# Kernel optimization log

Measured on AMD Instinct MI355X. Metric: run time of the kernel, lower is better.

## Reference

```python
import jax, jax.numpy as jnp
import numpy as np

B, T, DIM, HEADS, DH = 4, 2048, 1024, 16, 64  # dh = dim // heads


def setup_inputs() -> dict:
    key = jax.random.key(0)
    k1, k2, k3 = jax.random.split(key, 3)
    x = jax.random.normal(k1, (B, T, DIM), dtype=jnp.float32)
    # nn.Linear weights, stored as [in, out] for x @ W convention
    W_qkv = jax.random.normal(k2, (DIM, 3 * HEADS * DH), dtype=jnp.float32) * (DIM ** -0.5)
    W_o = jax.random.normal(k3, (HEADS * DH, DIM), dtype=jnp.float32) * ((HEADS * DH) ** -0.5)
    return {"x": x, "W_qkv": W_qkv, "W_o": W_o}


def reference(x, W_qkv, W_o):
    b, t, _ = x.shape
    qkv = x @ W_qkv  # [b, t, 3*h*dh]
    # einops 'b t (d k h) -> k b h t d' with k=3, h=HEADS: fused axis splits as (dh, 3, h)
    qkv = qkv.reshape(b, t, DH, 3, HEADS)
    qkv = jnp.transpose(qkv, (3, 0, 4, 1, 2))  # [3, b, h, t, dh]
    q, k, v = qkv[0], qkv[1], qkv[2]
    scale = DH ** -0.5
    scores = jnp.einsum('bhid,bhjd->bhij', q, k) * scale  # [b, h, t, t]
    attn = jax.nn.softmax(scores, axis=-1)
    out = jnp.einsum('bhij,bhjd->bhid', attn, v)  # [b, h, t, dh]
    out = jnp.transpose(out, (0, 2, 1, 3)).reshape(b, t, HEADS * DH)  # 'b h t d -> b t (h d)'
    return out @ W_o
```

## Files before the change

kernel.cpp:

```cpp
#include <hip/hip_runtime.h>

typedef __bf16 bf16;
typedef __bf16 bf16x2 __attribute__((ext_vector_type(2)));
typedef __bf16 bf16x4 __attribute__((ext_vector_type(4)));
typedef __bf16 bf16x8 __attribute__((ext_vector_type(8)));
typedef float  f32x4  __attribute__((ext_vector_type(4)));
typedef unsigned int u32;
typedef unsigned int u32x2 __attribute__((ext_vector_type(2)));
typedef unsigned int u32x4 __attribute__((ext_vector_type(4)));

#define LOG2E 1.44269504088896340736f
#define EXP_SC (0.125f * LOG2E)

#if __has_builtin(__builtin_amdgcn_exp2f)
#define EXP2F(x) __builtin_amdgcn_exp2f(x)
#else
#define EXP2F(x) __builtin_exp2f(x)
#endif

__device__ __forceinline__ u32 pk_bf16(float lo, float hi) {
  u32 a = __float_as_uint(lo) + 0x8000u;
  u32 b = __float_as_uint(hi) + 0x8000u;
  return __builtin_amdgcn_perm(b, a, 0x07060302);
}
#if __has_builtin(__builtin_amdgcn_cvt_pk_bf16_f32)
__device__ __forceinline__ u32 cvtpk(float lo, float hi) {
  bf16x2 t = __builtin_amdgcn_cvt_pk_bf16_f32(lo, hi);
  return __builtin_bit_cast(u32, t);
}
#else
__device__ __forceinline__ u32 cvtpk(float lo, float hi) { return pk_bf16(lo, hi); }
#endif
__device__ __forceinline__ unsigned short bf16r(float x) {
  return (unsigned short)((__float_as_uint(x) + 0x8000u) >> 16);
}

__device__ __forceinline__ void async_ld16(void* lds, const void* g) {
  __builtin_amdgcn_global_load_lds(
      (const __attribute__((address_space(1))) void*)(g),
      (__attribute__((address_space(3))) void*)(lds),
      16, 0, 0);
}

__global__ void prep_all(const float* __restrict__ x,    bf16* __restrict__ xb,
                         const float* __restrict__ Wqkv, bf16* __restrict__ wqkvT,
                         const float* __restrict__ Wo,   bf16* __restrict__ woT) {
  __shared__ float s[12288];
  const int bid = blockIdx.x;
  const int tid = threadIdx.x;
  if (bid < 8192) {
    int i = bid * 256 + tid;
    float4 v = ((const float4*)x)[i];
    u32x2 o = { pk_bf16(v.x, v.y), pk_bf16(v.z, v.w) };
    *(u32x2*)(xb + (size_t)i * 4) = o;
  } else if (bid < 8448) {
    const int k0 = (bid - 8192) * 4;
    for (int i = tid; i < 3072; i += 256) {
      int r = i / 768, c = (i - r * 768) * 4;
      *(float4*)(s + r * 3072 + c) = *(const float4*)(Wqkv + (size_t)(k0 + r) * 3072 + c);
    }
    __syncthreads();
    for (int n = tid; n < 3072; n += 256) {
      int d = n & 63, h = (n >> 6) & 15, wch = n >> 10;
      int on = d * 48 + wch * 16 + h;
      u32x2 v = { pk_bf16(s[0 * 3072 + on], s[1 * 3072 + on]),
                  pk_bf16(s[2 * 3072 + on], s[3 * 3072 + on]) };
      *(u32x2*)(wqkvT + (size_t)n * 1024 + k0) = v;
    }
  } else {
    const int k0 = (bid - 8448) * 8;
    for (int i = tid; i < 2048; i += 256) {
      int r = i >> 8, c = (i & 255) * 4;
      *(float4*)(s + r * 1024 + c) = *(const float4*)(Wo + (size_t)(k0 + r) * 1024 + c);
    }
    __syncthreads();
    for (int n = tid; n < 1024; n += 256) {
      u32x4 v = { pk_bf16(s[0 * 1024 + n], s[1 * 1024 + n]),
                  pk_bf16(s[2 * 1024 + n], s[3 * 1024 + n]),
                  pk_bf16(s[4 * 1024 + n], s[5 * 1024 + n]),
                  pk_bf16(s[6 * 1024 + n], s[7 * 1024 + n]) };
      *(u32x4*)(woT + (size_t)n * 1024 + k0) = v;
    }
  }
}

template <int MODE>
__launch_bounds__(256, 2)
__global__ void gemm_bt(const bf16* __restrict__ A, const bf16* __restrict__ BT,
                        float* __restrict__ C, int N,
                        bf16* __restrict__ Qb, bf16* __restrict__ Kb, bf16* __restrict__ Vb) {
  constexpr int K = 1024;
  __shared__ bf16 sA[128 * 64];
  __shared__ bf16 sB[128 * 64];
  const int m0 = blockIdx.x * 128;
  const int n0 = blockIdx.y * 128;
  const int tid = threadIdx.x;
  const int lane = tid & 63;
  const int w = tid >> 6;
  const int wm = (w >> 1) * 64, wn = (w & 1) * 64;
  const int l15 = lane & 15, quad = lane >> 4;

  f32x4 acc[4][4];
  for (int i = 0; i < 4; i++)
    for (int j = 0; j < 4; j++) acc[i][j] = f32x4{0.f, 0.f, 0.f, 0.f};

  const int rT = tid >> 3;
  const int jT = (tid & 7) ^ (rT & 7);
  const bf16* gA = A  + (size_t)(m0 + rT) * K + jT * 8;
  const bf16* gB = BT + (size_t)(n0 + rT) * K + jT * 8;

  for (int k0 = 0; k0 < K; k0 += 64) {
    __syncthreads();
    for (int i = 0; i < 4; i++) {
      async_ld16((void*)(sA + (i * 256 + w * 64) * 8), gA + (size_t)i * 32 * K);
      async_ld16((void*)(sB + (i * 256 + w * 64) * 8), gB + (size_t)i * 32 * K);
    }
    gA += 64; gB += 64;
    __syncthreads();

    for (int kk = 0; kk < 2; kk++) {
      bf16x8 af[4], bfr[4];
      for (int ms = 0; ms < 4; ms++) {
        int r = wm + ms * 16 + l15;
        af[ms] = *(const bf16x8*)(sA + r * 64 + (((kk * 4 + quad) ^ (r & 7)) * 8));
      }
      for (int ns = 0; ns < 4; ns++) {
        int r = wn + ns * 16 + l15;
        bfr[ns] = *(const bf16x8*)(sB + r * 64 + (((kk * 4 + quad) ^ (r & 7)) * 8));
      }
      for (int ms = 0; ms < 4; ms++)
        for (int ns = 0; ns < 4; ns++)
          acc[ms][ns] = __builtin_amdgcn_mfma_f32_16x16x32_bf16(af[ms], bfr[ns], acc[ms][ns], 0, 0, 0);
    }
  }

  if (MODE == 0) {
    for (int ms = 0; ms < 4; ms++)
      for (int ns = 0; ns < 4; ns++)
        for (int r = 0; r < 4; r++) {
          int row = m0 + wm + ms * 16 + quad * 4 + r;
          int col = n0 + wn + ns * 16 + l15;
          C[(size_t)row * N + col] = acc[ms][ns][r];
        }
  } else {
    for (int ms = 0; ms < 4; ms++)
      for (int ns = 0; ns < 4; ns++)
        for (int r = 0; r < 4; r++) {
          int row = m0 + wm + ms * 16 + quad * 4 + r;
          int col = n0 + wn + ns * 16 + l15;
          int b = row >> 11, t = row & 2047;
          int d = col & 63, h = (col >> 6) & 15, wch = col >> 10;
          bf16* dst = (wch == 0) ? Qb : (wch == 1) ? Kb : Vb;
          float v = acc[ms][ns][r] * ((wch == 0) ? EXP_SC : 1.0f);
          ((unsigned short*)dst)[(((size_t)(b * 16 + h)) * 2048 + t) * 64 + d] = bf16r(v);
        }
  }
}

__global__ void transpose_v(const bf16* __restrict__ V, bf16* __restrict__ VT) {
  __shared__ bf16 s[64 * 66];
  const int bh = blockIdx.y;
  const int t0 = blockIdx.x * 64;
  for (int i = threadIdx.x; i < 512; i += 256) {
    int t = i >> 3, dc = (i & 7) * 8;
    bf16x8 v = *(const bf16x8*)(V + ((size_t)bh * 2048 + t0 + t) * 64 + dc);
    for (int j = 0; j < 8; j++) s[t * 66 + dc + j] = v[j];
  }
  __syncthreads();
  for (int i = threadIdx.x; i < 512; i += 256) {
    int d = i >> 3, tc = (i & 7) * 8;
    bf16x8 v;
    for (int j = 0; j < 8; j++) {
      int kp = tc + j;
      int src = ((kp & 3) * 16) + (kp >> 2);
      v[j] = s[src * 66 + d];
    }
    *(bf16x8*)(VT + ((size_t)bh * 64 + d) * 2048 + t0 + tc) = v;
  }
}

__launch_bounds__(256, 2)
__global__ void attn_fwd(const bf16* __restrict__ Q, const bf16* __restrict__ K,
                         const bf16* __restrict__ VT, bf16* __restrict__ O) {
  __shared__ bf16 sK[64 * 64];
  __shared__ bf16 sV[64 * 64];
  __shared__ bf16 sP[4][32 * 64];
  const int bh = blockIdx.x;
  const int q0 = blockIdx.y * 128;
  const int tid = threadIdx.x;
  const int lane = tid & 63, w = tid >> 6;
  const int l15 = lane & 15, quad = lane >> 4;

  bf16x8 qf[2][2];
  for (int ms = 0; ms < 2; ms++)
    for (int kk = 0; kk < 2; kk++)
      qf[ms][kk] = *(const bf16x8*)(Q + ((size_t)bh * 2048 + q0 + w * 32 + ms * 16 + l15) * 64 + kk * 32 + quad * 8);

  f32x4 oa[2][4], lacc[2];
  for (int ms = 0; ms < 2; ms++) {
    for (int ds = 0; ds < 4; ds++) oa[ms][ds] = f32x4{0.f, 0.f, 0.f, 0.f};
    lacc[ms] = f32x4{0.f, 0.f, 0.f, 0.f};
  }
  bf16x8 onesf;
  for (int i = 0; i < 8; i++) onesf[i] = (bf16)1.0f;

  const int cA = w * 128 + lane;
  const int cB = cA + 64;
  const int rA = cA >> 3, jA = (cA & 7) ^ (rA & 7);
  const int rB = cB >> 3, jB = (cB & 7) ^ (rB & 7);
  const bf16* gKA = K  + ((size_t)bh * 2048 + rA) * 64 + jA * 8;
  const bf16* gKB = K  + ((size_t)bh * 2048 + rB) * 64 + jB * 8;
  const bf16* gVA = VT + ((size_t)bh * 64 + rA) * 2048 + jA * 8;
  const bf16* gVB = VT + ((size_t)bh * 64 + rB) * 2048 + jB * 8;

  int kvo[4][2], pfo[2][2], pwo[2][4];
  for (int ns = 0; ns < 4; ns++)
    for (int kk = 0; kk < 2; kk++) {
      int r = ns * 16 + l15;
      kvo[ns][kk] = r * 64 + (((kk * 4 + quad) ^ (r & 7)) * 8);
    }
  for (int ms = 0; ms < 2; ms++) {
    int r = ms * 16 + l15;
    for (int kk = 0; kk < 2; kk++)
      pfo[ms][kk] = r * 64 + (((kk * 4 + quad) ^ (r & 7)) * 8);
    for (int rr = 0; rr < 4; rr++) {
      int row = ms * 16 + quad * 4 + rr;
      pwo[ms][rr] = row * 64 + (((l15 >> 1) ^ (row & 7)) * 8) + (l15 & 1) * 4;
    }
  }

  for (int kt = 0; kt < 2048; kt += 64) {
    __syncthreads();
    async_ld16((void*)(sK + w * 1024),       gKA);
    async_ld16((void*)(sV + w * 1024),       gVA);
    async_ld16((void*)(sK + w * 1024 + 512), gKB);
    async_ld16((void*)(sV + w * 1024 + 512), gVB);
    gKA += 4096; gKB += 4096; gVA += 64; gVB += 64;
    __syncthreads();

    bf16x8 kf[4][2];
    for (int ns = 0; ns < 4; ns++)
      for (int kk = 0; kk < 2; kk++)
        kf[ns][kk] = *(const bf16x8*)(sK + kvo[ns][kk]);
    for (int ms = 0; ms < 2; ms++) {
      f32x4 s[4];
      for (int ns = 0; ns < 4; ns++) {
        f32x4 t = f32x4{0.f, 0.f, 0.f, 0.f};
        t = __builtin_amdgcn_mfma_f32_16x16x32_bf16(qf[ms][0], kf[ns][0], t, 0, 0, 0);
        t = __builtin_amdgcn_mfma_f32_16x16x32_bf16(qf[ms][1], kf[ns][1], t, 0, 0, 0);
        s[ns] = t;
      }
      for (int r = 0; r < 4; r++) {
        u32x2 pk = { cvtpk(EXP2F(s[0][r]), EXP2F(s[1][r])),
                     cvtpk(EXP2F(s[2][r]), EXP2F(s[3][r])) };
        *(u32x2*)(sP[w] + pwo[ms][r]) = pk;
      }
    }

    bf16x8 vf[4][2];
    for (int ds = 0; ds < 4; ds++)
      for (int kk = 0; kk < 2; kk++)
        vf[ds][kk] = *(const bf16x8*)(sV + kvo[ds][kk]);
    for (int ms = 0; ms < 2; ms++) {
      bf16x8 pf0 = *(const bf16x8*)(sP[w] + pfo[ms][0]);
      bf16x8 pf1 = *(const bf16x8*)(sP[w] + pfo[ms][1]);
      lacc[ms] = __builtin_amdgcn_mfma_f32_16x16x32_bf16(pf0, onesf, lacc[ms], 0, 0, 0);
      lacc[ms] = __builtin_amdgcn_mfma_f32_16x16x32_bf16(pf1, onesf, lacc[ms], 0, 0, 0);
      for (int ds = 0; ds < 4; ds++) {
        oa[ms][ds] = __builtin_amdgcn_mfma_f32_16x16x32_bf16(pf0, vf[ds][0], oa[ms][ds], 0, 0, 0);
        oa[ms][ds] = __builtin_amdgcn_mfma_f32_16x16x32_bf16(pf1, vf[ds][1], oa[ms][ds], 0, 0, 0);
      }
    }
  }

  const int b = bh >> 4, h = bh & 15;
  for (int ms = 0; ms < 2; ms++)
    for (int r = 0; r < 4; r++) {
      float inv = 1.0f / lacc[ms][r];
      int t = q0 + w * 32 + ms * 16 + quad * 4 + r;
      for (int ds = 0; ds < 4; ds++)
        ((unsigned short*)O)[((size_t)b * 2048 + t) * 1024 + h * 64 + ds * 16 + l15] =
            bf16r(oa[ms][ds][r] * inv);
    }
}

extern "C" void kernel_launch(void* const* d_in, const int* in_sizes, int n_in,
                              void* d_out, int out_size, void* d_ws, size_t ws_size,
                              hipStream_t stream) {
  const float* x    = (const float*)d_in[0];
  const float* Wqkv = (const float*)d_in[1];
  const float* Wo   = (const float*)d_in[2];
  float* out = (float*)d_out;
  char* ws = (char*)d_ws;

  bf16* wqkvT = (bf16*)(ws);
  bf16* woT   = (bf16*)(ws + 6291456);
  bf16* xb    = (bf16*)(ws + 8388608);
  bf16* Qb    = (bf16*)(ws + 25165824);
  bf16* Kb    = (bf16*)(ws + 41943040);
  bf16* Vb    = (bf16*)(ws + 58720256);
  bf16* VTb   = xb;
  bf16* AOb   = Vb;

  prep_all<<<8576, 256, 0, stream>>>(x, xb, Wqkv, wqkvT, Wo, woT);
  gemm_bt<1><<<dim3(64, 24), 256, 0, stream>>>(xb, wqkvT, nullptr, 3072, Qb, Kb, Vb);
  transpose_v<<<dim3(32, 64), 256, 0, stream>>>(Vb, VTb);
  attn_fwd<<<dim3(64, 16), 256, 0, stream>>>(Qb, Kb, VTb, AOb);
  gemm_bt<0><<<dim3(64, 8), 256, 0, stream>>>(AOb, woT, out, 1024, nullptr, nullptr, nullptr);
}
```

Before: 268.7 us.

## Software-pipeline attention loop across QK, exp, and PV stages with ring-buffered V

Restructures the attention main loop into a three-stage software pipeline. QK^T for tile t, exp of tile t-1 and PV for tile t-2 now run in the same iteration, with V in a 4-deep shared ring and P double-buffered per wave. Async loads of the next K/V tile are issued right after K fragments are read, to overlap global loads with compute. The row-sum moves from a ones-vector MFMA to a scalar accumulation finished with cross-lane shuffles. This uses more LDS (V ring and doubled P), which may cut occupancy below the two blocks per CU in launch_bounds, and it adds register pressure.

```diff
diff --git a/kernel.cpp b/kernel.cpp
--- a/kernel.cpp
+++ b/kernel.cpp
@@ -183,8 +183,8 @@
 __global__ void attn_fwd(const bf16* __restrict__ Q, const bf16* __restrict__ K,
                          const bf16* __restrict__ VT, bf16* __restrict__ O) {
   __shared__ bf16 sK[64 * 64];
-  __shared__ bf16 sV[64 * 64];
-  __shared__ bf16 sP[4][32 * 64];
+  __shared__ bf16 sV[4][64 * 64];
+  __shared__ bf16 sP[4][2][32 * 64];
   const int bh = blockIdx.x;
   const int q0 = blockIdx.y * 128;
   const int tid = threadIdx.x;
@@ -196,22 +196,17 @@
     for (int kk = 0; kk < 2; kk++)
       qf[ms][kk] = *(const bf16x8*)(Q + ((size_t)bh * 2048 + q0 + w * 32 + ms * 16 + l15) * 64 + kk * 32 + quad * 8);
 
-  f32x4 oa[2][4], lacc[2];
+  f32x4 oa[2][4];
+  float rs[2][4];
   for (int ms = 0; ms < 2; ms++) {
     for (int ds = 0; ds < 4; ds++) oa[ms][ds] = f32x4{0.f, 0.f, 0.f, 0.f};
-    lacc[ms] = f32x4{0.f, 0.f, 0.f, 0.f};
-  }
-  bf16x8 onesf;
-  for (int i = 0; i < 8; i++) onesf[i] = (bf16)1.0f;
+    for (int r = 0; r < 4; r++) rs[ms][r] = 0.f;
+  }
 
   const int cA = w * 128 + lane;
-  const int cB = cA + 64;
   const int rA = cA >> 3, jA = (cA & 7) ^ (rA & 7);
-  const int rB = cB >> 3, jB = (cB & 7) ^ (rB & 7);
-  const bf16* gKA = K  + ((size_t)bh * 2048 + rA) * 64 + jA * 8;
-  const bf16* gKB = K  + ((size_t)bh * 2048 + rB) * 64 + jB * 8;
-  const bf16* gVA = VT + ((size_t)bh * 64 + rA) * 2048 + jA * 8;
-  const bf16* gVB = VT + ((size_t)bh * 64 + rB) * 2048 + jB * 8;
+  const bf16* gK = K  + ((size_t)bh * 2048 + rA) * 64 + jA * 8;
+  const bf16* gV = VT + ((size_t)bh * 64 + rA) * 2048 + jA * 8;
 
   int kvo[4][2], pfo[2][2], pwo[2][4];
   for (int ns = 0; ns < 4; ns++)
@@ -229,57 +224,85 @@
     }
   }
 
-  for (int kt = 0; kt < 2048; kt += 64) {
-    __syncthreads();
-    async_ld16((void*)(sK + w * 1024),       gKA);
-    async_ld16((void*)(sV + w * 1024),       gVA);
-    async_ld16((void*)(sK + w * 1024 + 512), gKB);
-    async_ld16((void*)(sV + w * 1024 + 512), gVB);
-    gKA += 4096; gKB += 4096; gVA += 64; gVB += 64;
-    __syncthreads();
-
+  auto do_exp = [&](f32x4 (&Sp)[2][4], bf16* pw) {
+    for (int ms = 0; ms < 2; ms++)
+      for (int r = 0; r < 4; r++) {
+        float e0 = EXP2F(Sp[ms][0][r]), e1 = EXP2F(Sp[ms][1][r]);
+        float e2 = EXP2F(Sp[ms][2][r]), e3 = EXP2F(Sp[ms][3][r]);
+        rs[ms][r] += (e0 + e1) + (e2 + e3);
+        u32x2 pk = { cvtpk(e0, e1), cvtpk(e2, e3) };
+        *(u32x2*)(pw + pwo[ms][r]) = pk;
+      }
+  };
+  auto do_pv = [&](const bf16* pb, const bf16* vb) {
+    bf16x8 vf[4][2];
+    for (int ds = 0; ds < 4; ds++)
+      for (int kk = 0; kk < 2; kk++)
+        vf[ds][kk] = *(const bf16x8*)(vb + kvo[ds][kk]);
+    for (int ms = 0; ms < 2; ms++) {
+      bf16x8 pf0 = *(const bf16x8*)(pb + pfo[ms][0]);
+      bf16x8 pf1 = *(const bf16x8*)(pb + pfo[ms][1]);
+      for (int ds = 0; ds < 4; ds++) {
+        oa[ms][ds] = __builtin_amdgcn_mfma_f32_16x16x32_bf16(pf0, vf[ds][0], oa[ms][ds], 0, 0, 0);
+        oa[ms][ds] = __builtin_amdgcn_mfma_f32_16x16x32_bf16(pf1, vf[ds][1], oa[ms][ds], 0, 0, 0);
+      }
+    }
+  };
+
+  async_ld16((void*)(sK + w * 1024),            gK);
+  async_ld16((void*)(sK + w * 1024 + 512),      gK + 512);
+  async_ld16((void*)(sV[0] + w * 1024),         gV);
+  async_ld16((void*)(sV[0] + w * 1024 + 512),   gV + 16384);
+  gK += 4096; gV += 64;
+
+  f32x4 SA[2][4], SB[2][4];
+
+  auto step = [&](int t, f32x4 (&Sc)[2][4], f32x4 (&Sp)[2][4]) {
+    __syncthreads();
     bf16x8 kf[4][2];
     for (int ns = 0; ns < 4; ns++)
       for (int kk = 0; kk < 2; kk++)
         kf[ns][kk] = *(const bf16x8*)(sK + kvo[ns][kk]);
-    for (int ms = 0; ms < 2; ms++) {
-      f32x4 s[4];
+    __syncthreads();
+    if (t < 31) {
+      bf16* vb = sV[(t + 1) & 3];
+      async_ld16((void*)(sK + w * 1024),          gK);
+      async_ld16((void*)(sK + w * 1024 + 512),    gK + 512);
+      async_ld16((void*)(vb + w * 1024),          gV);
+      async_ld16((void*)(vb + w * 1024 + 512),    gV + 16384);
+      gK += 4096; gV += 64;
+    }
+    for (int ms = 0; ms < 2; ms++)
       for (int ns = 0; ns < 4; ns++) {
-        f32x4 t = f32x4{0.f, 0.f, 0.f, 0.f};
-        t = __builtin_amdgcn_mfma_f32_16x16x32_bf16(qf[ms][0], kf[ns][0], t, 0, 0, 0);
-        t = __builtin_amdgcn_mfma_f32_16x16x32_bf16(qf[ms][1], kf[ns][1], t, 0, 0, 0);
-        s[ns] = t;
-      }
-      for (int r = 0; r < 4; r++) {
-        u32x2 pk = { cvtpk(EXP2F(s[0][r]), EXP2F(s[1][r])),
-                     cvtpk(EXP2F(s[2][r]), EXP2F(s[3][r])) };
-        *(u32x2*)(sP[w] + pwo[ms][r]) = pk;
-      }
-    }
-
-    bf16x8 vf[4][2];
-    for (int ds = 0; ds < 4; ds++)
-      for (int kk = 0; kk < 2; kk++)
-        vf[ds][kk] = *(const bf16x8*)(sV + kvo[ds][kk]);
-    for (int ms = 0; ms < 2; ms++) {
-      bf16x8 pf0 = *(const bf16x8*)(sP[w] + pfo[ms][0]);
-      bf16x8 pf1 = *(const bf16x8*)(sP[w] + pfo[ms][1]);
-      lacc[ms] = __builtin_amdgcn_mfma_f32_16x16x32_bf16(pf0, onesf, lacc[ms], 0, 0, 0);
-      lacc[ms] = __builtin_amdgcn_mfma_f32_16x16x32_bf16(pf1, onesf, lacc[ms], 0, 0, 0);
-      for (int ds = 0; ds < 4; ds++) {
-        oa[ms][ds] = __builtin_amdgcn_mfma_f32_16x16x32_bf16(pf0, vf[ds][0], oa[ms][ds], 0, 0, 0);
-        oa[ms][ds] = __builtin_amdgcn_mfma_f32_16x16x32_bf16(pf1, vf[ds][1], oa[ms][ds], 0, 0, 0);
-      }
-    }
-  }
+        f32x4 acc0 = f32x4{0.f, 0.f, 0.f, 0.f};
+        acc0 = __builtin_amdgcn_mfma_f32_16x16x32_bf16(qf[ms][0], kf[ns][0], acc0, 0, 0, 0);
+        acc0 = __builtin_amdgcn_mfma_f32_16x16x32_bf16(qf[ms][1], kf[ns][1], acc0, 0, 0, 0);
+        Sc[ms][ns] = acc0;
+      }
+    if (t >= 1) do_exp(Sp, sP[w][(t - 1) & 1]);
+    if (t >= 2) do_pv(sP[w][t & 1], sV[(t - 2) & 3]);
+  };
+
+  for (int t = 0; t < 32; t += 2) {
+    step(t, SA, SB);
+    step(t + 1, SB, SA);
+  }
+  do_exp(SB, sP[w][1]);
+  do_pv(sP[w][0], sV[2]);
+  do_pv(sP[w][1], sV[3]);
 
   const int b = bh >> 4, h = bh & 15;
   for (int ms = 0; ms < 2; ms++)
     for (int r = 0; r < 4; r++) {
-      float inv = 1.0f / lacc[ms][r];
-      int t = q0 + w * 32 + ms * 16 + quad * 4 + r;
+      float t = rs[ms][r];
+      t += __shfl_xor(t, 1, 64);
+      t += __shfl_xor(t, 2, 64);
+      t += __shfl_xor(t, 4, 64);
+      t += __shfl_xor(t, 8, 64);
+      float inv = 1.0f / t;
+      int tq = q0 + w * 32 + ms * 16 + quad * 4 + r;
       for (int ds = 0; ds < 4; ds++)
-        ((unsigned short*)O)[((size_t)b * 2048 + t) * 1024 + h * 64 + ds * 16 + l15] =
+        ((unsigned short*)O)[((size_t)b * 2048 + tq) * 1024 + h * 64 + ds * 16 + l15] =
             bf16r(oa[ms][ds][r] * inv);
     }
 }
```

New measurement: 265.2 us. About the same (-1.3%).
